# Kernel tuning notes

Hardware: AMD Instinct MI355X
Metric: run time of the kernel (lower is better)

Reference implementation:

```python
import jax, jax.numpy as jnp
import numpy as np

LOG2 = float(np.log(2.0))


def setup_inputs() -> dict:
    key = jax.random.key(0)
    k1, k2 = jax.random.split(key)
    N, M = 65536, 1024
    logits = jax.random.normal(k1, (N, M), dtype=jnp.float32)
    true_class_idx = jax.random.randint(k2, (N,), 0, M, dtype=jnp.int64)
    return {"logits": logits, "true_class_idx": true_class_idx}


def reference(logits, true_class_idx):
    # logits: [N, M]; true_class_idx: [N]
    n, m = logits.shape
    true_logits = jnp.take_along_axis(logits, true_class_idx[:, None], axis=1)[:, 0]  # [N]
    # sum_k logaddexp(false_k, true) over the m-1 false classes.
    # Compute over all m classes, then subtract the k==true term, which equals
    # logaddexp(true, true) = true + log(2).
    pairwise = jnp.logaddexp(logits, true_logits[:, None])  # [N, M]
    logsum = pairwise.sum(axis=1) - (true_logits + LOG2)  # [N]
    tuplemax_loss = logsum / (m - 1) - true_logits  # [N]
    return tuplemax_loss.mean()
```

## Files before the change

kernel.cpp:

```cpp
#include <hip/hip_runtime.h>

#define LN2F      0.69314718055994530942f
#define LOG2EF    1.44269504088896340736f

__device__ __forceinline__ float laexp_terms(float x, float t, float& s_hi, float& s_lg) {
    float hi = fmaxf(x, t);
    float lo = fminf(x, t);
    float e  = __builtin_amdgcn_exp2f((lo - hi) * LOG2EF);
    s_hi += hi;
    s_lg += __builtin_amdgcn_logf(1.0f + e);
    return hi;
}

__global__ __launch_bounds__(256) void tuplemax_loss_1024(
    const float* __restrict__ logits,
    const int*   __restrict__ true_idx,
    float*       __restrict__ out,
    int n)
{
    const int lane            = threadIdx.x & 63;
    const int wid             = threadIdx.x >> 6;
    const int gwave           = blockIdx.x * 4 + wid;
    const int nwaves          = gridDim.x * 4;

    float acc = 0.0f;

    for (int row = gwave; row < n; row += nwaves) {
        const int   tidx = true_idx[row];
        const float t    = logits[(size_t)row * 1024 + tidx];
        const float4* rowp = (const float4*)(logits + (size_t)row * 1024) + lane;

        float4 v0 = rowp[0];
        float4 v1 = rowp[64];
        float4 v2 = rowp[128];
        float4 v3 = rowp[192];

        float s_hi = 0.0f, s_lg = 0.0f;
        #pragma unroll
        for (int j = 0; j < 4; ++j) laexp_terms((&v0.x)[j], t, s_hi, s_lg);
        #pragma unroll
        for (int j = 0; j < 4; ++j) laexp_terms((&v1.x)[j], t, s_hi, s_lg);
        #pragma unroll
        for (int j = 0; j < 4; ++j) laexp_terms((&v2.x)[j], t, s_hi, s_lg);
        #pragma unroll
        for (int j = 0; j < 4; ++j) laexp_terms((&v3.x)[j], t, s_hi, s_lg);

        float s = fmaf(s_lg, LN2F, s_hi);

        #pragma unroll
        for (int off = 32; off >= 1; off >>= 1)
            s += __shfl_xor(s, off, 64);

        if (lane == 0) {
            float logsum = s - (t + LN2F);
            acc += logsum * (1.0f / 1023.0f) - t;
        }
    }

    __shared__ float partial[4];
    if (lane == 0) partial[wid] = acc;
    __syncthreads();
    if (threadIdx.x == 0) {
        float s = partial[0] + partial[1] + partial[2] + partial[3];
        atomicAdd(out, s * (1.0f / (float)n));
    }
}

__global__ __launch_bounds__(256) void tuplemax_loss_generic(
    const float* __restrict__ logits,
    const int*   __restrict__ true_idx,
    float*       __restrict__ out,
    int n, int m)
{
    const int lane   = threadIdx.x & 63;
    const int wid    = threadIdx.x >> 6;
    const int gwave  = blockIdx.x * 4 + wid;
    const int nwaves = gridDim.x * 4;
    const int m4     = m >> 2;

    float acc = 0.0f;

    for (int row = gwave; row < n; row += nwaves) {
        const int   tidx = true_idx[row];
        const float t    = logits[(size_t)row * m + tidx];
        const float4* rowp = (const float4*)(logits + (size_t)row * m);

        float s_hi = 0.0f, s_lg = 0.0f;
        for (int k4 = lane; k4 < m4; k4 += 64) {
            float4 v = rowp[k4];
            #pragma unroll
            for (int j = 0; j < 4; ++j) laexp_terms((&v.x)[j], t, s_hi, s_lg);
        }
        float s = fmaf(s_lg, LN2F, s_hi);

        #pragma unroll
        for (int off = 32; off >= 1; off >>= 1)
            s += __shfl_xor(s, off, 64);

        if (lane == 0) {
            float logsum = s - (t + LN2F);
            acc += logsum / (float)(m - 1) - t;
        }
    }

    __shared__ float partial[4];
    if (lane == 0) partial[wid] = acc;
    __syncthreads();
    if (threadIdx.x == 0) {
        float s = partial[0] + partial[1] + partial[2] + partial[3];
        atomicAdd(out, s * (1.0f / (float)n));
    }
}

extern "C" void kernel_launch(void* const* d_in, const int* in_sizes, int n_in,
                              void* d_out, int out_size, void* d_ws, size_t ws_size,
                              hipStream_t stream) {
    const float* logits = (const float*)d_in[0];
    const int*   tidx   = (const int*)d_in[1];
    float*       out    = (float*)d_out;

    const int n = in_sizes[1];
    const int m = in_sizes[0] / n;

    hipMemsetAsync(out, 0, sizeof(float), stream);

    const int block = 256;
    const int grid  = 2048;
    if (m == 1024) {
        tuplemax_loss_1024<<<grid, block, 0, stream>>>(logits, tidx, out, n);
    } else {
        tuplemax_loss_generic<<<grid, block, 0, stream>>>(logits, tidx, out, n, m);
    }
}
```

Before: 356.0 us.

## Process eight rows per wave with double-buffered row loads and one reduction

The 1024-column kernel now gives each wave a fixed block of eight consecutive rows instead of grid-striding. It loads the eight true indices with vector loads and prefetches the next row's float4s while the current row is computed, so global-load latency overlaps with the exp/log work. The per-row cross-lane shuffle reduction is replaced by a single reduction per wave, with the true-logit and log2 corrections folded in algebraically. The grid becomes n/32 blocks, which assumes n is divisible by 32; other shapes fall back to the generic kernel.

```diff
diff --git a/kernel.cpp b/kernel.cpp
--- a/kernel.cpp
+++ b/kernel.cpp
@@ -1,15 +1,26 @@
 #include <hip/hip_runtime.h>
 
-#define LN2F      0.69314718055994530942f
-#define LOG2EF    1.44269504088896340736f
+#define LN2F   0.69314718055994530942f
+#define LOG2EF 1.44269504088896340736f
 
-__device__ __forceinline__ float laexp_terms(float x, float t, float& s_hi, float& s_lg) {
+__device__ __forceinline__ void laexp1(float x, float t, float& s_hi, float& s_lg) {
     float hi = fmaxf(x, t);
     float lo = fminf(x, t);
-    float e  = __builtin_amdgcn_exp2f((lo - hi) * LOG2EF);
     s_hi += hi;
-    s_lg += __builtin_amdgcn_logf(1.0f + e);
-    return hi;
+    s_lg += __builtin_amdgcn_logf(1.0f + __builtin_amdgcn_exp2f((lo - hi) * LOG2EF));
+}
+
+__device__ __forceinline__ void laexp16(const float4& q0, const float4& q1,
+                                        const float4& q2, const float4& q3,
+                                        float t, float& s_hi, float& s_lg) {
+    laexp1(q0.x, t, s_hi, s_lg); laexp1(q0.y, t, s_hi, s_lg);
+    laexp1(q0.z, t, s_hi, s_lg); laexp1(q0.w, t, s_hi, s_lg);
+    laexp1(q1.x, t, s_hi, s_lg); laexp1(q1.y, t, s_hi, s_lg);
+    laexp1(q1.z, t, s_hi, s_lg); laexp1(q1.w, t, s_hi, s_lg);
+    laexp1(q2.x, t, s_hi, s_lg); laexp1(q2.y, t, s_hi, s_lg);
+    laexp1(q2.z, t, s_hi, s_lg); laexp1(q2.w, t, s_hi, s_lg);
+    laexp1(q3.x, t, s_hi, s_lg); laexp1(q3.y, t, s_hi, s_lg);
+    laexp1(q3.z, t, s_hi, s_lg); laexp1(q3.w, t, s_hi, s_lg);
 }
 
 __global__ __launch_bounds__(256) void tuplemax_loss_1024(
@@ -18,47 +29,58 @@
     float*       __restrict__ out,
     int n)
 {
-    const int lane            = threadIdx.x & 63;
-    const int wid             = threadIdx.x >> 6;
-    const int gwave           = blockIdx.x * 4 + wid;
-    const int nwaves          = gridDim.x * 4;
+    const int lane = threadIdx.x & 63;
+    const int wid  = threadIdx.x >> 6;
+    const int w    = blockIdx.x * 4 + wid;
+    const int row0 = w * 8;
 
-    float acc = 0.0f;
+    const float* base = logits + (size_t)row0 * 1024;
 
-    for (int row = gwave; row < n; row += nwaves) {
-        const int   tidx = true_idx[row];
-        const float t    = logits[(size_t)row * 1024 + tidx];
-        const float4* rowp = (const float4*)(logits + (size_t)row * 1024) + lane;
+#define LOADR(Q0, Q1, Q2, Q3, K) do {                                   \
+        const float4* rp = (const float4*)(base + ((size_t)(K) << 10)) + lane; \
+        Q0 = rp[0]; Q1 = rp[64]; Q2 = rp[128]; Q3 = rp[192];            \
+    } while (0)
 
-        float4 v0 = rowp[0];
-        float4 v1 = rowp[64];
-        float4 v2 = rowp[128];
-        float4 v3 = rowp[192];
+    float4 a0, a1, a2, a3, b0, b1, b2, b3;
+    LOADR(a0, a1, a2, a3, 0);
+    LOADR(b0, b1, b2, b3, 1);
 
-        float s_hi = 0.0f, s_lg = 0.0f;
-        #pragma unroll
-        for (int j = 0; j < 4; ++j) laexp_terms((&v0.x)[j], t, s_hi, s_lg);
-        #pragma unroll
-        for (int j = 0; j < 4; ++j) laexp_terms((&v1.x)[j], t, s_hi, s_lg);
-        #pragma unroll
-        for (int j = 0; j < 4; ++j) laexp_terms((&v2.x)[j], t, s_hi, s_lg);
-        #pragma unroll
-        for (int j = 0; j < 4; ++j) laexp_terms((&v3.x)[j], t, s_hi, s_lg);
+    const int4 ia = *(const int4*)(true_idx + row0);
+    const int4 ib = *(const int4*)(true_idx + row0 + 4);
 
-        float s = fmaf(s_lg, LN2F, s_hi);
+    float tv[8];
+    tv[0] = base[(0 << 10) + ia.x];
+    tv[1] = base[(1 << 10) + ia.y];
+    tv[2] = base[(2 << 10) + ia.z];
+    tv[3] = base[(3 << 10) + ia.w];
+    tv[4] = base[(4 << 10) + ib.x];
+    tv[5] = base[(5 << 10) + ib.y];
+    tv[6] = base[(6 << 10) + ib.z];
+    tv[7] = base[(7 << 10) + ib.w];
 
-        #pragma unroll
-        for (int off = 32; off >= 1; off >>= 1)
-            s += __shfl_xor(s, off, 64);
+    float s_hi = 0.0f, s_lg = 0.0f, tsum = 0.0f;
 
-        if (lane == 0) {
-            float logsum = s - (t + LN2F);
-            acc += logsum * (1.0f / 1023.0f) - t;
-        }
+    #pragma unroll
+    for (int k = 0; k < 8; k += 2) {
+        tsum += tv[k] + tv[k + 1];
+        laexp16(a0, a1, a2, a3, tv[k], s_hi, s_lg);
+        if (k + 2 < 8) LOADR(a0, a1, a2, a3, k + 2);
+        laexp16(b0, b1, b2, b3, tv[k + 1], s_hi, s_lg);
+        if (k + 3 < 8) LOADR(b0, b1, b2, b3, k + 3);
     }
+#undef LOADR
+
+    float S = fmaf(s_lg, LN2F, s_hi);
+    #pragma unroll
+    for (int off = 32; off >= 1; off >>= 1)
+        S += __shfl_xor(S, off, 64);
 
     __shared__ float partial[4];
-    if (lane == 0) partial[wid] = acc;
+    if (lane == 0) {
+        partial[wid] = S * (1.0f / 1023.0f)
+                     - tsum * (1024.0f / 1023.0f)
+                     - 8.0f * LN2F * (1.0f / 1023.0f);
+    }
     __syncthreads();
     if (threadIdx.x == 0) {
         float s = partial[0] + partial[1] + partial[2] + partial[3];
@@ -79,7 +101,6 @@
     const int m4     = m >> 2;
 
     float acc = 0.0f;
-
     for (int row = gwave; row < n; row += nwaves) {
         const int   tidx = true_idx[row];
         const float t    = logits[(size_t)row * m + tidx];
@@ -88,15 +109,13 @@
         float s_hi = 0.0f, s_lg = 0.0f;
         for (int k4 = lane; k4 < m4; k4 += 64) {
             float4 v = rowp[k4];
-            #pragma unroll
-            for (int j = 0; j < 4; ++j) laexp_terms((&v.x)[j], t, s_hi, s_lg);
+            laexp1(v.x, t, s_hi, s_lg); laexp1(v.y, t, s_hi, s_lg);
+            laexp1(v.z, t, s_hi, s_lg); laexp1(v.w, t, s_hi, s_lg);
         }
         float s = fmaf(s_lg, LN2F, s_hi);
-
         #pragma unroll
         for (int off = 32; off >= 1; off >>= 1)
             s += __shfl_xor(s, off, 64);
-
         if (lane == 0) {
             float logsum = s - (t + LN2F);
             acc += logsum / (float)(m - 1) - t;
@@ -124,11 +143,10 @@
 
     hipMemsetAsync(out, 0, sizeof(float), stream);
 
-    const int block = 256;
-    const int grid  = 2048;
-    if (m == 1024) {
-        tuplemax_loss_1024<<<grid, block, 0, stream>>>(logits, tidx, out, n);
+    if (m == 1024 && (n % 32) == 0) {
+        const int grid = n / 32;
+        tuplemax_loss_1024<<<grid, 256, 0, stream>>>(logits, tidx, out, n);
     } else {
-        tuplemax_loss_generic<<<grid, block, 0, stream>>>(logits, tidx, out, n, m);
+        tuplemax_loss_generic<<<2048, 256, 0, stream>>>(logits, tidx, out, n, m);
     }
 }
```

Measured after the change: 355.0 us, median of 2. About the same (-0.3%).
